# Kernel optimization log

Hardware: AMD Instinct MI355X
Metric: run time of the kernel (lower is better)

## Reference

```python
import jax, jax.numpy as jnp
import numpy as np

DIM = 256
NUM_HEADS = 8
HEAD_DIM = DIM // NUM_HEADS  # 32
WINDOW = 8
SCALE = HEAD_DIM ** -0.5


def setup_inputs() -> dict:
    key = jax.random.key(0)
    k_x, k_wq, k_bq, k_wp, k_bp = jax.random.split(key, 5)
    x = jax.random.normal(k_x, (16, DIM, 128, 128), dtype=jnp.float32)
    # torch nn.Linear weights: [out_features, in_features]
    w_qkv = jax.random.normal(k_wq, (3 * DIM, DIM), dtype=jnp.float32) * (DIM ** -0.5)
    b_qkv = jax.random.normal(k_bq, (3 * DIM,), dtype=jnp.float32) * 0.02
    w_proj = jax.random.normal(k_wp, (DIM, DIM), dtype=jnp.float32) * (DIM ** -0.5)
    b_proj = jax.random.normal(k_bp, (DIM,), dtype=jnp.float32) * 0.02
    return {"x": x, "w_qkv": w_qkv, "b_qkv": b_qkv, "w_proj": w_proj, "b_proj": b_proj}


def _attend(tokens, w_qkv, b_qkv, w_proj, b_proj):
    # tokens: [N, T, C]
    N, T, C = tokens.shape
    qkv = tokens @ w_qkv.T + b_qkv                      # [N, T, 3C]
    qkv = qkv.reshape(N, T, 3, NUM_HEADS, HEAD_DIM)
    q, k, v = qkv[:, :, 0], qkv[:, :, 1], qkv[:, :, 2]  # [N, T, h, d]
    attn = jnp.einsum('nqhd,nkhd->nhqk', q, k) * SCALE  # [N, h, T, T]
    attn = jax.nn.softmax(attn, axis=-1)
    out = jnp.einsum('nhqk,nkhd->nqhd', attn, v).reshape(N, T, C)
    return out @ w_proj.T + b_proj


def reference(x, w_qkv, b_qkv, w_proj, b_proj):
    B, C, H, W = x.shape
    w = WINDOW
    Hn, Wn = H // w, W // w
    # partition into windows: [B, C, H, W] -> [B*Hn*Wn, w*w, C]
    xw = x.reshape(B, C, Hn, w, Wn, w)
    xw = xw.transpose(0, 2, 4, 3, 5, 1).reshape(B * Hn * Wn, w * w, C)
    out = _attend(xw, w_qkv, b_qkv, w_proj, b_proj)
    # reassemble: [B*Hn*Wn, w*w, C] -> [B, C, H, W]
    out = out.reshape(B, Hn, Wn, w, w, C)
    out = out.transpose(0, 5, 1, 3, 2, 4).reshape(B, C, H, W)
    return out
```

## Files before the change

### kernel.cpp

```cpp
#include <hip/hip_runtime.h>

typedef _Float16 f16x8 __attribute__((ext_vector_type(8)));
typedef _Float16 f16x4 __attribute__((ext_vector_type(4)));
typedef float f32x4 __attribute__((ext_vector_type(4)));

#define A_STRIDE 264
#define LDS_BYTES (64 * A_STRIDE * 2)

__device__ __forceinline__ float packh2(float x, float y) {
  union { float f; _Float16 h[2]; } u;
  u.h[0] = (_Float16)x; u.h[1] = (_Float16)y;
  return u.f;
}

__device__ __forceinline__ f16x8 regroup(float lo0, float lo1, float hi0, float hi1,
                                         int c16, int q) {
  int sA = c16 | ((q & 1) << 5);
  int sB = sA | 16;
  float a0 = __shfl(lo0, sA), a1 = __shfl(lo1, sA);
  float a2 = __shfl(hi0, sA), a3 = __shfl(hi1, sA);
  float b0 = __shfl(lo0, sB), b1 = __shfl(lo1, sB);
  float b2 = __shfl(hi0, sB), b3 = __shfl(hi1, sB);
  bool hi = q >= 2;
  float4 f;
  f.x = hi ? a2 : a0; f.y = hi ? a3 : a1;
  f.z = hi ? b2 : b0; f.w = hi ? b3 : b1;
  union { float4 v; f16x8 h; } u; u.v = f;
  return u.h;
}

__global__ __launch_bounds__(256) void convert_weights_kernel(
    const float* __restrict__ wqkv, const float* __restrict__ wproj,
    _Float16* __restrict__ dst) {
  int i = blockIdx.x * 256 + threadIdx.x;
  float4 v;
  if (i < 49152) v = ((const float4*)wqkv)[i];
  else           v = ((const float4*)wproj)[i - 49152];
  f16x4 h;
  h[0] = (_Float16)v.x; h[1] = (_Float16)v.y;
  h[2] = (_Float16)v.z; h[3] = (_Float16)v.w;
  *(f16x4*)&dst[4 * i] = h;
}

__global__ __launch_bounds__(512, 4) void win_attn_kernel(
    const float* __restrict__ x, const _Float16* __restrict__ Wh,
    const float* __restrict__ bqkv, const float* __restrict__ bproj,
    float* __restrict__ out)
{
  __shared__ __align__(16) char smem[LDS_BYTES];
  _Float16* A = (_Float16*)smem;

  const int tid  = threadIdx.x;
  const int lane = tid & 63;
  const int wv   = tid >> 6;
  const int c16  = lane & 15;
  const int q    = lane >> 4;

  const int id = blockIdx.x;
  const int g = id >> 4, s = id & 15;
  const int w = (g << 4) | ((s & 7) << 1) | (s >> 3);
  const int b  = w >> 8;
  const int hn = (w >> 4) & 15;
  const int wn = w & 15;
  const size_t xbase = (size_t)b * (256 * 16384) + (size_t)(hn * 8) * 128 + (size_t)(wn * 8);

  {
    const int pq = lane >> 4;
    const int i  = (lane >> 1) & 7;
    const int jj = lane & 1;
    const size_t sp = xbase + (size_t)i * 128 + jj * 4;
    #pragma unroll
    for (int ss = 0; ss < 4; ++ss) {
      int c = wv * 32 + (ss * 4 + pq) * 2;
      float4 v0 = *(const float4*)&x[sp + (size_t)c * 16384];
      float4 v1 = *(const float4*)&x[sp + (size_t)(c + 1) * 16384];
      int t0 = i * 8 + jj * 4;
      *(float*)&A[(t0 + 0) * A_STRIDE + c] = packh2(v0.x, v1.x);
      *(float*)&A[(t0 + 1) * A_STRIDE + c] = packh2(v0.y, v1.y);
      *(float*)&A[(t0 + 2) * A_STRIDE + c] = packh2(v0.z, v1.z);
      *(float*)&A[(t0 + 3) * A_STRIDE + c] = packh2(v0.w, v1.w);
    }
  }
  __syncthreads();

  f16x8 vf[2][2];
  {
    f32x4 av[4][2];
    #pragma unroll
    for (int mu = 0; mu < 4; ++mu)
      #pragma unroll
      for (int nd = 0; nd < 2; ++nd)
        av[mu][nd] = (f32x4){0.f,0.f,0.f,0.f};
    const _Float16* Wv = Wh + (size_t)(512 + 32 * wv) * 256;
    __builtin_amdgcn_s_setprio(1);
    #pragma unroll
    for (int k0 = 0; k0 < 8; ++k0) {
      f16x8 xf[4];
      #pragma unroll
      for (int mu = 0; mu < 4; ++mu)
        xf[mu] = *(const f16x8*)&A[(mu * 16 + c16) * A_STRIDE + k0 * 32 + q * 8];
      f16x8 wv0 = *(const f16x8*)&Wv[(c16) * 256 + k0 * 32 + q * 8];
      f16x8 wv1 = *(const f16x8*)&Wv[(16 + c16) * 256 + k0 * 32 + q * 8];
      #pragma unroll
      for (int mu = 0; mu < 4; ++mu) {
        av[mu][0] = __builtin_amdgcn_mfma_f32_16x16x32_f16(xf[mu], wv0, av[mu][0], 0, 0, 0);
        av[mu][1] = __builtin_amdgcn_mfma_f32_16x16x32_f16(xf[mu], wv1, av[mu][1], 0, 0, 0);
      }
    }
    __builtin_amdgcn_s_setprio(0);
    #pragma unroll
    for (int nd = 0; nd < 2; ++nd) {
      float bv = bqkv[512 + 32 * wv + nd * 16 + c16];
      #pragma unroll
      for (int mu = 0; mu < 4; ++mu) {
        av[mu][nd][0] += bv; av[mu][nd][1] += bv; av[mu][nd][2] += bv; av[mu][nd][3] += bv;
      }
      float pv[4][2];
      #pragma unroll
      for (int mu = 0; mu < 4; ++mu) {
        pv[mu][0] = packh2(av[mu][nd][0], av[mu][nd][1]);
        pv[mu][1] = packh2(av[mu][nd][2], av[mu][nd][3]);
      }
      #pragma unroll
      for (int kk = 0; kk < 2; ++kk)
        vf[nd][kk] = regroup(pv[2*kk][0], pv[2*kk][1], pv[2*kk+1][0], pv[2*kk+1][1], c16, q);
    }
  }

  f16x8 qf[4], kf[4];
  #pragma unroll
  for (int pass = 0; pass < 2; ++pass) {
    f32x4 ac[2][4];
    #pragma unroll
    for (int md = 0; md < 2; ++md)
      #pragma unroll
      for (int nt = 0; nt < 4; ++nt)
        ac[md][nt] = (f32x4){0.f,0.f,0.f,0.f};
    const _Float16* Wx = Wh + (size_t)(256 * pass + 32 * wv) * 256;
    __builtin_amdgcn_s_setprio(1);
    #pragma unroll
    for (int k0 = 0; k0 < 8; ++k0) {
      f16x8 xf[4];
      #pragma unroll
      for (int nt = 0; nt < 4; ++nt)
        xf[nt] = *(const f16x8*)&A[(nt * 16 + c16) * A_STRIDE + k0 * 32 + q * 8];
      f16x8 w0 = *(const f16x8*)&Wx[(c16) * 256 + k0 * 32 + q * 8];
      f16x8 w1 = *(const f16x8*)&Wx[(16 + c16) * 256 + k0 * 32 + q * 8];
      #pragma unroll
      for (int nt = 0; nt < 4; ++nt) {
        ac[0][nt] = __builtin_amdgcn_mfma_f32_16x16x32_f16(w0, xf[nt], ac[0][nt], 0, 0, 0);
        ac[1][nt] = __builtin_amdgcn_mfma_f32_16x16x32_f16(w1, xf[nt], ac[1][nt], 0, 0, 0);
      }
    }
    __builtin_amdgcn_s_setprio(0);
    #pragma unroll
    for (int md = 0; md < 2; ++md) {
      float4 bb = *(const float4*)&bqkv[256 * pass + 32 * wv + md * 16 + 4 * q];
      #pragma unroll
      for (int nt = 0; nt < 4; ++nt) {
        ac[md][nt][0] += bb.x; ac[md][nt][1] += bb.y;
        ac[md][nt][2] += bb.z; ac[md][nt][3] += bb.w;
      }
    }
    #pragma unroll
    for (int nt = 0; nt < 4; ++nt) {
      f16x8 f = regroup(packh2(ac[0][nt][0], ac[0][nt][1]), packh2(ac[0][nt][2], ac[0][nt][3]),
                        packh2(ac[1][nt][0], ac[1][nt][1]), packh2(ac[1][nt][2], ac[1][nt][3]),
                        c16, q);
      if (pass == 0) qf[nt] = f; else kf[nt] = f;
    }
  }

  f32x4 O[2][4];
  float rinv[4];
  {
    const float kExpScale = 0.25506973288423525f;
    #pragma unroll
    for (int nt = 0; nt < 4; ++nt) {
      f32x4 S[4];
      __builtin_amdgcn_s_setprio(1);
      #pragma unroll
      for (int mu = 0; mu < 4; ++mu)
        S[mu] = __builtin_amdgcn_mfma_f32_16x16x32_f16(
            kf[mu], qf[nt], (f32x4){0.f,0.f,0.f,0.f}, 0, 0, 0);
      __builtin_amdgcn_s_setprio(0);

      float mx = S[0][0];
      #pragma unroll
      for (int mu = 0; mu < 4; ++mu)
        #pragma unroll
        for (int r = 0; r < 4; ++r)
          mx = fmaxf(mx, S[mu][r]);
      mx = fmaxf(mx, __shfl_xor(mx, 16));
      mx = fmaxf(mx, __shfl_xor(mx, 32));
      float sum = 0.f;
      #pragma unroll
      for (int mu = 0; mu < 4; ++mu)
        #pragma unroll
        for (int r = 0; r < 4; ++r) {
          float e = exp2f((S[mu][r] - mx) * kExpScale);
          S[mu][r] = e; sum += e;
        }
      sum += __shfl_xor(sum, 16);
      sum += __shfl_xor(sum, 32);
      rinv[nt] = 1.0f / sum;

      float pp[4][2];
      #pragma unroll
      for (int mu = 0; mu < 4; ++mu) {
        pp[mu][0] = packh2(S[mu][0], S[mu][1]);
        pp[mu][1] = packh2(S[mu][2], S[mu][3]);
      }
      O[0][nt] = (f32x4){0.f,0.f,0.f,0.f};
      O[1][nt] = (f32x4){0.f,0.f,0.f,0.f};
      #pragma unroll
      for (int kk = 0; kk < 2; ++kk) {
        f16x8 pf = regroup(pp[2*kk][0], pp[2*kk][1], pp[2*kk+1][0], pp[2*kk+1][1], c16, q);
        __builtin_amdgcn_s_setprio(1);
        O[0][nt] = __builtin_amdgcn_mfma_f32_16x16x32_f16(vf[0][kk], pf, O[0][nt], 0, 0, 0);
        O[1][nt] = __builtin_amdgcn_mfma_f32_16x16x32_f16(vf[1][kk], pf, O[1][nt], 0, 0, 0);
        __builtin_amdgcn_s_setprio(0);
      }
    }
  }

  __syncthreads();
  {
    #pragma unroll
    for (int md = 0; md < 2; ++md)
      #pragma unroll
      for (int nt = 0; nt < 4; ++nt) {
        int t = nt * 16 + c16;
        int c = 32 * wv + md * 16 + 4 * q;
        *(float*)&A[t * A_STRIDE + c]     = packh2(O[md][nt][0] * rinv[nt], O[md][nt][1] * rinv[nt]);
        *(float*)&A[t * A_STRIDE + c + 2] = packh2(O[md][nt][2] * rinv[nt], O[md][nt][3] * rinv[nt]);
      }
  }
  __syncthreads();

  {
    f32x4 ap[2][4];
    #pragma unroll
    for (int me = 0; me < 2; ++me)
      #pragma unroll
      for (int nt = 0; nt < 4; ++nt)
        ap[me][nt] = (f32x4){0.f,0.f,0.f,0.f};
    const _Float16* Wp = Wh + (size_t)768 * 256 + (size_t)(32 * wv) * 256;
    __builtin_amdgcn_s_setprio(1);
    #pragma unroll
    for (int k0 = 0; k0 < 8; ++k0) {
      f16x8 af[4];
      #pragma unroll
      for (int nt = 0; nt < 4; ++nt)
        af[nt] = *(const f16x8*)&A[(nt * 16 + c16) * A_STRIDE + k0 * 32 + q * 8];
      f16x8 wp0 = *(const f16x8*)&Wp[(c16) * 256 + k0 * 32 + q * 8];
      f16x8 wp1 = *(const f16x8*)&Wp[(16 + c16) * 256 + k0 * 32 + q * 8];
      #pragma unroll
      for (int nt = 0; nt < 4; ++nt) {
        ap[0][nt] = __builtin_amdgcn_mfma_f32_16x16x32_f16(wp0, af[nt], ap[0][nt], 0, 0, 0);
        ap[1][nt] = __builtin_amdgcn_mfma_f32_16x16x32_f16(wp1, af[nt], ap[1][nt], 0, 0, 0);
      }
    }
    __builtin_amdgcn_s_setprio(0);
    #pragma unroll
    for (int me = 0; me < 2; ++me) {
      float4 bp = *(const float4*)&bproj[32 * wv + me * 16 + 4 * q];
      #pragma unroll
      for (int nt = 0; nt < 4; ++nt) {
        int t = nt * 16 + c16;
        size_t sp = xbase + (size_t)(t >> 3) * 128 + (t & 7);
        int e = 32 * wv + me * 16 + 4 * q;
        out[sp + (size_t)(e + 0) * 16384] = ap[me][nt][0] + bp.x;
        out[sp + (size_t)(e + 1) * 16384] = ap[me][nt][1] + bp.y;
        out[sp + (size_t)(e + 2) * 16384] = ap[me][nt][2] + bp.z;
        out[sp + (size_t)(e + 3) * 16384] = ap[me][nt][3] + bp.w;
      }
    }
  }
}

extern "C" void kernel_launch(void* const* d_in, const int* in_sizes, int n_in,
                              void* d_out, int out_size, void* d_ws, size_t ws_size,
                              hipStream_t stream) {
  (void)in_sizes; (void)n_in; (void)out_size; (void)ws_size;
  const float* x     = (const float*)d_in[0];
  const float* wqkv  = (const float*)d_in[1];
  const float* bqkv  = (const float*)d_in[2];
  const float* wproj = (const float*)d_in[3];
  const float* bproj = (const float*)d_in[4];
  float* out = (float*)d_out;
  _Float16* Wh = (_Float16*)d_ws;

  hipLaunchKernelGGL(convert_weights_kernel, dim3(256), dim3(256), 0, stream,
                     wqkv, wproj, Wh);
  hipLaunchKernelGGL(win_attn_kernel, dim3(4096), dim3(512), 0, stream,
                     x, Wh, bqkv, bproj, out);
}
```

Baseline: 724.4 us.

## Process four windows per block with double-buffered LDS and register prefetch of x

Each block now handles four consecutive windows along a row instead of one, with the grid cut to 1024 blocks. The next window's x tile is loaded into registers during attention and written to a second LDS buffer after the projection. This hides global-load latency behind compute and amortises block launch cost. The channel-pair order of the x-to-LDS staging is also rotated per row to reduce LDS bank conflicts. In exchange LDS doubles (about 67 KB per block), which may lower occupancy, register pressure rises from the prefetch buffer, and there are fewer blocks to spread across CUs.

```diff
diff --git a/kernel.cpp b/kernel.cpp
--- a/kernel.cpp
+++ b/kernel.cpp
@@ -5,7 +5,8 @@
 typedef float f32x4 __attribute__((ext_vector_type(4)));
 
 #define A_STRIDE 264
-#define LDS_BYTES (64 * A_STRIDE * 2)
+#define A_BYTES (64 * A_STRIDE * 2)
+#define WPB 4
 
 __device__ __forceinline__ float packh2(float x, float y) {
   union { float f; _Float16 h[2]; } u;
@@ -42,45 +43,42 @@
   *(f16x4*)&dst[4 * i] = h;
 }
 
-__global__ __launch_bounds__(512, 4) void win_attn_kernel(
+__device__ __forceinline__ void load_x_regs(const float* __restrict__ x, size_t xw,
+                                            int wv, int lane, float4 (&nx)[8]) {
+  const int pq = lane >> 4, i = (lane >> 1) & 7, jj = lane & 1;
+  const size_t sp = xw + (size_t)i * 128 + (size_t)(jj * 4);
+  #pragma unroll
+  for (int ss = 0; ss < 4; ++ss) {
+    int cp = (ss * 4 + pq + 2 * i) & 15;
+    int c  = wv * 32 + cp * 2;
+    nx[2 * ss]     = *(const float4*)&x[sp + (size_t)c * 16384];
+    nx[2 * ss + 1] = *(const float4*)&x[sp + (size_t)(c + 1) * 16384];
+  }
+}
+
+__device__ __forceinline__ void store_x_lds(_Float16* __restrict__ A,
+                                            int wv, int lane, const float4 (&nx)[8]) {
+  const int pq = lane >> 4, i = (lane >> 1) & 7, jj = lane & 1;
+  #pragma unroll
+  for (int ss = 0; ss < 4; ++ss) {
+    int cp = (ss * 4 + pq + 2 * i) & 15;
+    int c  = wv * 32 + cp * 2;
+    int t0 = i * 8 + jj * 4;
+    float4 v0 = nx[2 * ss], v1 = nx[2 * ss + 1];
+    *(float*)&A[(t0 + 0) * A_STRIDE + c] = packh2(v0.x, v1.x);
+    *(float*)&A[(t0 + 1) * A_STRIDE + c] = packh2(v0.y, v1.y);
+    *(float*)&A[(t0 + 2) * A_STRIDE + c] = packh2(v0.z, v1.z);
+    *(float*)&A[(t0 + 3) * A_STRIDE + c] = packh2(v0.w, v1.w);
+  }
+}
+
+__device__ __forceinline__ void process_window(
     const float* __restrict__ x, const _Float16* __restrict__ Wh,
     const float* __restrict__ bqkv, const float* __restrict__ bproj,
-    float* __restrict__ out)
+    float* __restrict__ out, _Float16* __restrict__ Acur,
+    _Float16* __restrict__ Anext, size_t xw, size_t xw_next, bool pf,
+    int lane, int wv, int c16, int q, float4 (&nx)[8])
 {
-  __shared__ __align__(16) char smem[LDS_BYTES];
-  _Float16* A = (_Float16*)smem;
-
-  const int tid  = threadIdx.x;
-  const int lane = tid & 63;
-  const int wv   = tid >> 6;
-  const int c16  = lane & 15;
-  const int q    = lane >> 4;
-
-  const int id = blockIdx.x;
-  const int g = id >> 4, s = id & 15;
-  const int w = (g << 4) | ((s & 7) << 1) | (s >> 3);
-  const int b  = w >> 8;
-  const int hn = (w >> 4) & 15;
-  const int wn = w & 15;
-  const size_t xbase = (size_t)b * (256 * 16384) + (size_t)(hn * 8) * 128 + (size_t)(wn * 8);
-
-  {
-    const int pq = lane >> 4;
-    const int i  = (lane >> 1) & 7;
-    const int jj = lane & 1;
-    const size_t sp = xbase + (size_t)i * 128 + jj * 4;
-    #pragma unroll
-    for (int ss = 0; ss < 4; ++ss) {
-      int c = wv * 32 + (ss * 4 + pq) * 2;
-      float4 v0 = *(const float4*)&x[sp + (size_t)c * 16384];
-      float4 v1 = *(const float4*)&x[sp + (size_t)(c + 1) * 16384];
-      int t0 = i * 8 + jj * 4;
-      *(float*)&A[(t0 + 0) * A_STRIDE + c] = packh2(v0.x, v1.x);
-      *(float*)&A[(t0 + 1) * A_STRIDE + c] = packh2(v0.y, v1.y);
-      *(float*)&A[(t0 + 2) * A_STRIDE + c] = packh2(v0.z, v1.z);
-      *(float*)&A[(t0 + 3) * A_STRIDE + c] = packh2(v0.w, v1.w);
-    }
-  }
   __syncthreads();
 
   f16x8 vf[2][2];
@@ -98,7 +96,7 @@
       f16x8 xf[4];
       #pragma unroll
       for (int mu = 0; mu < 4; ++mu)
-        xf[mu] = *(const f16x8*)&A[(mu * 16 + c16) * A_STRIDE + k0 * 32 + q * 8];
+        xf[mu] = *(const f16x8*)&Acur[(mu * 16 + c16) * A_STRIDE + k0 * 32 + q * 8];
       f16x8 wv0 = *(const f16x8*)&Wv[(c16) * 256 + k0 * 32 + q * 8];
       f16x8 wv1 = *(const f16x8*)&Wv[(16 + c16) * 256 + k0 * 32 + q * 8];
       #pragma unroll
@@ -143,7 +141,7 @@
       f16x8 xf[4];
       #pragma unroll
       for (int nt = 0; nt < 4; ++nt)
-        xf[nt] = *(const f16x8*)&A[(nt * 16 + c16) * A_STRIDE + k0 * 32 + q * 8];
+        xf[nt] = *(const f16x8*)&Acur[(nt * 16 + c16) * A_STRIDE + k0 * 32 + q * 8];
       f16x8 w0 = *(const f16x8*)&Wx[(c16) * 256 + k0 * 32 + q * 8];
       f16x8 w1 = *(const f16x8*)&Wx[(16 + c16) * 256 + k0 * 32 + q * 8];
       #pragma unroll
@@ -215,14 +213,16 @@
       O[1][nt] = (f32x4){0.f,0.f,0.f,0.f};
       #pragma unroll
       for (int kk = 0; kk < 2; ++kk) {
-        f16x8 pf = regroup(pp[2*kk][0], pp[2*kk][1], pp[2*kk+1][0], pp[2*kk+1][1], c16, q);
+        f16x8 pfr = regroup(pp[2*kk][0], pp[2*kk][1], pp[2*kk+1][0], pp[2*kk+1][1], c16, q);
         __builtin_amdgcn_s_setprio(1);
-        O[0][nt] = __builtin_amdgcn_mfma_f32_16x16x32_f16(vf[0][kk], pf, O[0][nt], 0, 0, 0);
-        O[1][nt] = __builtin_amdgcn_mfma_f32_16x16x32_f16(vf[1][kk], pf, O[1][nt], 0, 0, 0);
+        O[0][nt] = __builtin_amdgcn_mfma_f32_16x16x32_f16(vf[0][kk], pfr, O[0][nt], 0, 0, 0);
+        O[1][nt] = __builtin_amdgcn_mfma_f32_16x16x32_f16(vf[1][kk], pfr, O[1][nt], 0, 0, 0);
         __builtin_amdgcn_s_setprio(0);
       }
     }
   }
+
+  if (pf) load_x_regs(x, xw_next, wv, lane, nx);
 
   __syncthreads();
   {
@@ -232,8 +232,8 @@
       for (int nt = 0; nt < 4; ++nt) {
         int t = nt * 16 + c16;
         int c = 32 * wv + md * 16 + 4 * q;
-        *(float*)&A[t * A_STRIDE + c]     = packh2(O[md][nt][0] * rinv[nt], O[md][nt][1] * rinv[nt]);
-        *(float*)&A[t * A_STRIDE + c + 2] = packh2(O[md][nt][2] * rinv[nt], O[md][nt][3] * rinv[nt]);
+        *(float*)&Acur[t * A_STRIDE + c]     = packh2(O[md][nt][0] * rinv[nt], O[md][nt][1] * rinv[nt]);
+        *(float*)&Acur[t * A_STRIDE + c + 2] = packh2(O[md][nt][2] * rinv[nt], O[md][nt][3] * rinv[nt]);
       }
   }
   __syncthreads();
@@ -252,7 +252,7 @@
       f16x8 af[4];
       #pragma unroll
       for (int nt = 0; nt < 4; ++nt)
-        af[nt] = *(const f16x8*)&A[(nt * 16 + c16) * A_STRIDE + k0 * 32 + q * 8];
+        af[nt] = *(const f16x8*)&Acur[(nt * 16 + c16) * A_STRIDE + k0 * 32 + q * 8];
       f16x8 wp0 = *(const f16x8*)&Wp[(c16) * 256 + k0 * 32 + q * 8];
       f16x8 wp1 = *(const f16x8*)&Wp[(16 + c16) * 256 + k0 * 32 + q * 8];
       #pragma unroll
@@ -268,7 +268,7 @@
       #pragma unroll
       for (int nt = 0; nt < 4; ++nt) {
         int t = nt * 16 + c16;
-        size_t sp = xbase + (size_t)(t >> 3) * 128 + (t & 7);
+        size_t sp = xw + (size_t)(t >> 3) * 128 + (size_t)(t & 7);
         int e = 32 * wv + me * 16 + 4 * q;
         out[sp + (size_t)(e + 0) * 16384] = ap[me][nt][0] + bp.x;
         out[sp + (size_t)(e + 1) * 16384] = ap[me][nt][1] + bp.y;
@@ -276,6 +276,43 @@
         out[sp + (size_t)(e + 3) * 16384] = ap[me][nt][3] + bp.w;
       }
     }
+  }
+
+  if (pf) store_x_lds(Anext, wv, lane, nx);
+}
+
+__global__ __launch_bounds__(512, 4) void win_attn_kernel(
+    const float* __restrict__ x, const _Float16* __restrict__ Wh,
+    const float* __restrict__ bqkv, const float* __restrict__ bproj,
+    float* __restrict__ out)
+{
+  __shared__ __align__(16) char smem[2 * A_BYTES];
+  _Float16* A0 = (_Float16*)smem;
+  _Float16* A1 = (_Float16*)(smem + A_BYTES);
+
+  const int tid  = threadIdx.x;
+  const int lane = tid & 63;
+  const int wv   = tid >> 6;
+  const int c16  = lane & 15;
+  const int q    = lane >> 4;
+
+  const int B   = blockIdx.x;
+  const int bi  = B >> 6;
+  const int hn  = (B >> 2) & 15;
+  const int wn4 = B & 3;
+  const size_t xrow = (size_t)bi * (256 * 16384) + (size_t)(hn * 8) * 128 + (size_t)(wn4 * 32);
+
+  float4 nx[8];
+  load_x_regs(x, xrow, wv, lane, nx);
+  store_x_lds(A0, wv, lane, nx);
+
+  #pragma unroll 1
+  for (int ip = 0; ip < WPB / 2; ++ip) {
+    size_t xw0 = xrow + (size_t)(2 * ip) * 8;
+    process_window(x, Wh, bqkv, bproj, out, A0, A1, xw0, xw0 + 8, true,
+                   lane, wv, c16, q, nx);
+    process_window(x, Wh, bqkv, bproj, out, A1, A0, xw0 + 8, xw0 + 16,
+                   (2 * ip + 1) < (WPB - 1), lane, wv, c16, q, nx);
   }
 }
 
@@ -293,6 +330,6 @@
 
   hipLaunchKernelGGL(convert_weights_kernel, dim3(256), dim3(256), 0, stream,
                      wqkv, wproj, Wh);
-  hipLaunchKernelGGL(win_attn_kernel, dim3(4096), dim3(512), 0, stream,
+  hipLaunchKernelGGL(win_attn_kernel, dim3(1024), dim3(512), 0, stream,
                      x, Wh, bqkv, bproj, out);
 }
```

New measurement: 1.706 ms. 2.36x slower.
